# Optimization experiments

Hardware: AMD Instinct MI355X
Metric: run time of the kernel (lower is better)

Reference implementation:

```python
import jax, jax.numpy as jnp
import numpy as np

B, N, DIM, HEADS = 2048, 64, 256, 8
WH = WW = 8  # window size; N = WH*WW


def _buffers():
    # continuous relative coords table [1, 2*WH-1, 2*WW-1, 2], log-scaled as in Swin-V2
    rh = np.arange(-(WH - 1), WH, dtype=np.float32)
    rw = np.arange(-(WW - 1), WW, dtype=np.float32)
    t = np.stack(np.meshgrid(rh, rw, indexing='ij'), axis=-1)[None]
    t[..., 0] /= (WH - 1)
    t[..., 1] /= (WW - 1)
    t *= 8.0
    t = np.sign(t) * np.log2(np.abs(t) + 1.0) / np.log2(8.0)
    # relative position index [N, N]
    ch, cw = np.arange(WH), np.arange(WW)
    coords = np.stack(np.meshgrid(ch, cw, indexing='ij')).reshape(2, -1)
    rel = (coords[:, :, None] - coords[:, None, :]).transpose(1, 2, 0)
    rel[..., 0] += WH - 1
    rel[..., 1] += WW - 1
    rel[..., 0] *= 2 * WW - 1
    idx = rel.sum(-1)
    return jnp.asarray(t, dtype=jnp.float32), jnp.asarray(idx, dtype=jnp.int32)


def setup_inputs() -> dict:
    key = jax.random.key(0)
    ks = jax.random.split(key, 8)
    tbl, idx = _buffers()
    return {
        'x': jax.random.normal(ks[0], (B, N, DIM), dtype=jnp.float32),
        'qkv_w': jax.random.normal(ks[1], (3 * DIM, DIM), dtype=jnp.float32) * 0.02,
        'q_bias': jnp.zeros((DIM,), dtype=jnp.float32),
        'v_bias': jnp.zeros((DIM,), dtype=jnp.float32),
        'scale': jnp.full((HEADS, 1, 1), np.log(10.0), dtype=jnp.float32),
        'cpb_w1': jax.random.normal(ks[2], (512, 2), dtype=jnp.float32) * 0.02,
        'cpb_b1': jnp.zeros((512,), dtype=jnp.float32),
        'cpb_w2': jax.random.normal(ks[3], (HEADS, 512), dtype=jnp.float32) * 0.02,
        'proj_w': jax.random.normal(ks[4], (DIM, DIM), dtype=jnp.float32) * 0.02,
        'proj_b': jnp.zeros((DIM,), dtype=jnp.float32),
        'rel_coords_table': tbl,
        'rel_pos_index': idx,
    }


def reference(x, qkv_w, q_bias, v_bias, scale, cpb_w1, cpb_b1, cpb_w2,
              proj_w, proj_b, rel_coords_table, rel_pos_index):
    b, n, c = x.shape
    h = scale.shape[0]
    d = c // h
    # qkv projection, bias = [q_bias, 0, v_bias]
    bias = jnp.concatenate([q_bias, jnp.zeros_like(v_bias), v_bias])
    qkv = x @ qkv_w.T + bias
    q, k, v = jnp.split(qkv, 3, axis=-1)
    to_heads = lambda t: t.reshape(b, n, h, d).transpose(0, 2, 1, 3)  # b h n d
    q, k, v = to_heads(q), to_heads(k), to_heads(v)
    # cosine attention: L2-normalize q, k (F.normalize eps=1e-12)
    l2n = lambda t: t / jnp.maximum(jnp.linalg.norm(t, axis=-1, keepdims=True), 1e-12)
    q, k = l2n(q), l2n(k)
    attn = jnp.einsum('bhnd,bhmd->bhnm', q, k)
    # clamped learnable log-temperature per head
    sc = jnp.exp(jnp.minimum(scale, jnp.log(jnp.float32(100.0))))  # [h,1,1]
    attn = attn * sc
    # continuous position bias: MLP(2->512->h), gathered by rel index, 16*sigmoid
    tbl = jax.nn.relu(rel_coords_table @ cpb_w1.T + cpb_b1) @ cpb_w2.T  # [1,15,15,h]
    tbl = tbl.reshape(-1, h)
    cpb = tbl[rel_pos_index.reshape(-1)].reshape(n, n, h).transpose(2, 0, 1)  # [h,n,n]
    attn = attn + 16.0 * jax.nn.sigmoid(cpb)[None]
    attn = jax.nn.softmax(attn, axis=-1)
    out = jnp.einsum('bhnm,bhmd->bhnd', attn, v)
    out = out.transpose(0, 2, 1, 3).reshape(b, n, c)
    return out @ proj_w.T + proj_b
```

## Files before the change

### kernel.cpp

```cpp
#include <hip/hip_runtime.h>
#include <stdint.h>

typedef unsigned short u16;
typedef unsigned int u32;
typedef short bf8_t __attribute__((ext_vector_type(8)));
typedef float f4_t  __attribute__((ext_vector_type(4)));
typedef float f16_t __attribute__((ext_vector_type(16)));

#define LOG2E 1.44269504088896340736f

static __device__ __forceinline__ u32 pkbf(float lo, float hi){
  u32 r; asm("v_cvt_pk_bf16_f32 %0, %1, %2" : "=v"(r) : "v"(lo), "v"(hi)); return r;
}

static __device__ __forceinline__ float pair_add(float v, bool hi5){
  union { float f; u32 u; } a; a.f = v;
  auto r = __builtin_amdgcn_permlane32_swap(a.u, a.u, false, false);
  union { u32 u; float f; } p; p.u = hi5 ? r[0] : r[1];
  return v + p.f;
}

static __device__ __forceinline__ void cvt_tile(const f16_t c, bf8_t& f0, bf8_t& f1){
  u32 p0 = pkbf(c[0], c[1]),  p1 = pkbf(c[2], c[3]);
  u32 p2 = pkbf(c[4], c[5]),  p3 = pkbf(c[6], c[7]);
  u32 p4 = pkbf(c[8], c[9]),  p5 = pkbf(c[10], c[11]);
  u32 p6 = pkbf(c[12], c[13]), p7 = pkbf(c[14], c[15]);
  auto r02 = __builtin_amdgcn_permlane32_swap(p0, p2, false, false);
  auto r13 = __builtin_amdgcn_permlane32_swap(p1, p3, false, false);
  auto r46 = __builtin_amdgcn_permlane32_swap(p4, p6, false, false);
  auto r57 = __builtin_amdgcn_permlane32_swap(p5, p7, false, false);
  union { u32 u[4]; bf8_t b; } x0, x1;
  x0.u[0] = r02[0]; x0.u[1] = r13[0]; x0.u[2] = r02[1]; x0.u[3] = r13[1];
  x1.u[0] = r46[0]; x1.u[1] = r57[0]; x1.u[2] = r46[1]; x1.u[3] = r57[1];
  f0 = x0.b; f1 = x1.b;
}

#define MFMA32(a, b, c) __builtin_amdgcn_mfma_f32_32x32x16_bf16(a, b, c, 0, 0, 0)


__global__ __launch_bounds__(256)
void prep_kernel(const float* __restrict__ qkvw, const float* __restrict__ projw,
                 const float* __restrict__ tab, const float* __restrict__ w1,
                 const float* __restrict__ b1, const float* __restrict__ w2,
                 u16* __restrict__ wpk, float* __restrict__ tbl){
  __shared__ float red[4][8];
  if (blockIdx.x < 128){
    int u = blockIdx.x * 256 + threadIdx.x;
    int hb  = u >> 10;
    int ks  = (u >> 6) & 15;
    int l5  = (u >> 5) & 1;
    int l31 = u & 31;
    int row = hb * 32 + l31, col = ks * 16 + l5 * 8;
    const float* src = (row < 768) ? (qkvw + (size_t)row * 256 + col)
                                   : (projw + (size_t)(row - 768) * 256 + col);
    float4 v0 = *reinterpret_cast<const float4*>(src);
    float4 v1 = *reinterpret_cast<const float4*>(src + 4);
    uint4 p;
    p.x = pkbf(v0.x, v0.y); p.y = pkbf(v0.z, v0.w);
    p.z = pkbf(v1.x, v1.y); p.w = pkbf(v1.z, v1.w);
    *reinterpret_cast<uint4*>(wpk + (size_t)u * 8) = p;
  } else {
    int i = blockIdx.x - 128;
    int tid = threadIdx.x;
    int wv = tid >> 6, lane = tid & 63;
    float c0 = tab[2*i], c1 = tab[2*i+1];
    int j0 = tid * 2;
    float4 w14 = *reinterpret_cast<const float4*>(w1 + 2*j0);
    float2 b12 = *reinterpret_cast<const float2*>(b1 + j0);
    float h0 = fmaxf(fmaf(c1, w14.y, fmaf(c0, w14.x, b12.x)), 0.f);
    float h1 = fmaxf(fmaf(c1, w14.w, fmaf(c0, w14.z, b12.y)), 0.f);
    float part[8];
    #pragma unroll
    for (int hh = 0; hh < 8; hh++){
      float2 w22 = *reinterpret_cast<const float2*>(w2 + hh*512 + j0);
      part[hh] = fmaf(h1, w22.y, h0 * w22.x);
    }
    #pragma unroll
    for (int hh = 0; hh < 8; hh++)
      #pragma unroll
      for (int off = 1; off < 64; off <<= 1)
        part[hh] += __shfl_xor(part[hh], off);
    if (lane == 0){
      #pragma unroll
      for (int hh = 0; hh < 8; hh++) red[wv][hh] = part[hh];
    }
    __syncthreads();
    if (tid < 8)
      tbl[i*8 + tid] = (red[0][tid] + red[1][tid]) + (red[2][tid] + red[3][tid]);
  }
}

__global__ void cpbgather_kernel(const float* __restrict__ tbl, const int* __restrict__ idx,
                                 const float* __restrict__ scale, float* __restrict__ biasF,
                                 float* __restrict__ scf){
  int u = blockIdx.x * blockDim.x + threadIdx.x;
  int rl   = u & 3;
  int lane = (u >> 2) & 63;
  int r4   = (u >> 8) & 3;
  int tile = (u >> 10) & 3;
  int hh   = (u >> 12) & 7;
  int qt = tile & 1, kt = tile >> 1;
  int query = 32*qt + (lane & 31);
  int key   = 32*kt + rl + 8*r4 + 4*(lane >> 5);
  int id = idx[query*64 + key];
  float xv = tbl[id*8 + hh];
  float s = 1.f / (1.f + expf(-xv));
  float qsh = expf(fminf(scale[hh], 4.6051701859880913680f)) * LOG2E;
  biasF[u] = 16.f * s * LOG2E - (qsh + 24.0f);
  if (u < 8) scf[u] = qsh;
}

#define XS 264

__global__ __launch_bounds__(512, 4)
void winattn_kernel(const float* __restrict__ x, const u16* __restrict__ wpk,
                    const float* __restrict__ qb, const float* __restrict__ vbias,
                    const float* __restrict__ biasF, const float* __restrict__ scf,
                    const float* __restrict__ projb, float* __restrict__ out){
  __shared__ u16 xlds[64 * XS];
  __shared__ u16 olds[64 * XS];

  const int b = blockIdx.x;
  const int t = threadIdx.x;
  const int w = t >> 6, lane = t & 63;
  const int l31 = lane & 31, l5 = lane >> 5;
  const bool hi5 = (l5 != 0);
  const int h = w;
  const int fragoff = l5 * 256 + l31 * 8;

  {
    const f4_t* xg = reinterpret_cast<const f4_t*>(x + (size_t)b * 16384);
    #pragma unroll
    for (int i = 0; i < 8; i++){
      int fi = t + 512 * i;
      f4_t v = __builtin_nontemporal_load(xg + fi);
      uint2 p; p.x = pkbf(v[0], v[1]); p.y = pkbf(v[2], v[3]);
      *reinterpret_cast<uint2*>(&xlds[(fi >> 6) * XS + (fi & 63) * 4]) = p;
    }
  }
  __syncthreads();

  bf8_t qf0, qf1, qf2, qf3;
  bf8_t kf0, kf1, kf2, kf3;
  bf8_t vf0, vf1, vf2, vf3;
  const float qs = scf[h];

  {
    f16_t cq0, cq1;
    #pragma unroll
    for (int r = 0; r < 16; r++){
      float bqr = qb[32*h + (r & 3) + 8*(r >> 2) + 4*l5];
      cq0[r] = bqr; cq1[r] = bqr;
    }
    const u16* wqf = wpk + (size_t)h * 8192 + fragoff;
    __builtin_amdgcn_s_setprio(1);
    #pragma unroll 4
    for (int ks = 0; ks < 16; ks++){
      const int ko = ks * 16 + 8 * l5;
      bf8_t aq  = *reinterpret_cast<const bf8_t*>(wqf + ks * 512);
      bf8_t bx0 = *reinterpret_cast<const bf8_t*>(&xlds[l31 * XS + ko]);
      bf8_t bx1 = *reinterpret_cast<const bf8_t*>(&xlds[(32 + l31) * XS + ko]);
      cq0 = MFMA32(aq, bx0, cq0);
      cq1 = MFMA32(aq, bx1, cq1);
    }
    __builtin_amdgcn_s_setprio(0);
    {
      float sq = 0.f;
      #pragma unroll
      for (int r = 0; r < 16; r++) sq = fmaf(cq0[r], cq0[r], sq);
      sq = pair_add(sq, hi5);
      float iq = qs * __builtin_amdgcn_rsqf(fmaxf(sq, 1e-24f));
      #pragma unroll
      for (int r = 0; r < 16; r++) cq0[r] *= iq;
      cvt_tile(cq0, qf0, qf1);
    }
    {
      float sq = 0.f;
      #pragma unroll
      for (int r = 0; r < 16; r++) sq = fmaf(cq1[r], cq1[r], sq);
      sq = pair_add(sq, hi5);
      float iq = qs * __builtin_amdgcn_rsqf(fmaxf(sq, 1e-24f));
      #pragma unroll
      for (int r = 0; r < 16; r++) cq1[r] *= iq;
      cvt_tile(cq1, qf2, qf3);
    }
  }

  {
    f16_t ck0, ck1;
    #pragma unroll
    for (int r = 0; r < 16; r++){ ck0[r] = 0.f; ck1[r] = 0.f; }
    const u16* wkf = wpk + (size_t)(8 + h) * 8192 + fragoff;
    __builtin_amdgcn_s_setprio(1);
    #pragma unroll 4
    for (int ks = 0; ks < 16; ks++){
      const int ko = ks * 16 + 8 * l5;
      bf8_t ak  = *reinterpret_cast<const bf8_t*>(wkf + ks * 512);
      bf8_t bx0 = *reinterpret_cast<const bf8_t*>(&xlds[l31 * XS + ko]);
      bf8_t bx1 = *reinterpret_cast<const bf8_t*>(&xlds[(32 + l31) * XS + ko]);
      ck0 = MFMA32(ak, bx0, ck0);
      ck1 = MFMA32(ak, bx1, ck1);
    }
    __builtin_amdgcn_s_setprio(0);
    {
      float sk = 0.f;
      #pragma unroll
      for (int r = 0; r < 16; r++) sk = fmaf(ck0[r], ck0[r], sk);
      sk = pair_add(sk, hi5);
      float ik = __builtin_amdgcn_rsqf(fmaxf(sk, 1e-24f));
      #pragma unroll
      for (int r = 0; r < 16; r++) ck0[r] *= ik;
      cvt_tile(ck0, kf0, kf1);
    }
    {
      float sk = 0.f;
      #pragma unroll
      for (int r = 0; r < 16; r++) sk = fmaf(ck1[r], ck1[r], sk);
      sk = pair_add(sk, hi5);
      float ik = __builtin_amdgcn_rsqf(fmaxf(sk, 1e-24f));
      #pragma unroll
      for (int r = 0; r < 16; r++) ck1[r] *= ik;
      cvt_tile(ck1, kf2, kf3);
    }
  }

  {
    f16_t cv0, cv1;
    float bv = vbias[32*h + l31];
    #pragma unroll
    for (int r = 0; r < 16; r++){ cv0[r] = bv; cv1[r] = bv; }
    const u16* wvf = wpk + (size_t)(16 + h) * 8192 + fragoff;
    __builtin_amdgcn_s_setprio(1);
    #pragma unroll 4
    for (int ks = 0; ks < 16; ks++){
      const int ko = ks * 16 + 8 * l5;
      bf8_t bw  = *reinterpret_cast<const bf8_t*>(wvf + ks * 512);
      bf8_t ax0 = *reinterpret_cast<const bf8_t*>(&xlds[l31 * XS + ko]);
      bf8_t ax1 = *reinterpret_cast<const bf8_t*>(&xlds[(32 + l31) * XS + ko]);
      cv0 = MFMA32(ax0, bw, cv0);
      cv1 = MFMA32(ax1, bw, cv1);
    }
    __builtin_amdgcn_s_setprio(0);
    cvt_tile(cv0, vf0, vf1);
    cvt_tile(cv1, vf2, vf3);
  }

  #pragma unroll
  for (int nt = 0; nt < 2; nt++){
    union { f16_t c; f4_t q[4]; } S0, S1;
    {
      const f4_t* bf0 = reinterpret_cast<const f4_t*>(biasF) + (h*4 + nt    ) * 256 + lane;
      const f4_t* bf1 = reinterpret_cast<const f4_t*>(biasF) + (h*4 + 2 + nt) * 256 + lane;
      #pragma unroll
      for (int r4 = 0; r4 < 4; r4++){ S0.q[r4] = bf0[r4 * 64]; S1.q[r4] = bf1[r4 * 64]; }
    }
    f16_t s0 = S0.c, s1 = S1.c;
    bf8_t qfa = nt ? qf2 : qf0, qfb = nt ? qf3 : qf1;
    __builtin_amdgcn_s_setprio(1);
    s0 = MFMA32(kf0, qfa, s0); s0 = MFMA32(kf1, qfb, s0);
    s1 = MFMA32(kf2, qfa, s1); s1 = MFMA32(kf3, qfb, s1);
    __builtin_amdgcn_s_setprio(0);
    #pragma unroll
    for (int r = 0; r < 16; r++){
      s0[r] = __builtin_amdgcn_exp2f(s0[r]);
      s1[r] = __builtin_amdgcn_exp2f(s1[r]);
    }
    float a0 = 0.f, a1 = 0.f, a2 = 0.f, a3 = 0.f;
    #pragma unroll
    for (int r4 = 0; r4 < 4; r4++){
      a0 += s0[4*r4 + 0] + s1[4*r4 + 0];
      a1 += s0[4*r4 + 1] + s1[4*r4 + 1];
      a2 += s0[4*r4 + 2] + s1[4*r4 + 2];
      a3 += s0[4*r4 + 3] + s1[4*r4 + 3];
    }
    float ssum = pair_add((a0 + a1) + (a2 + a3), hi5);
    float invr = __builtin_amdgcn_rcpf(ssum);
    bf8_t pf0, pf1, pf2, pf3;
    cvt_tile(s0, pf0, pf1);
    cvt_tile(s1, pf2, pf3);
    f16_t co;
    #pragma unroll
    for (int r = 0; r < 16; r++) co[r] = 0.f;
    __builtin_amdgcn_s_setprio(1);
    co = MFMA32(vf0, pf0, co); co = MFMA32(vf1, pf1, co);
    co = MFMA32(vf2, pf2, co); co = MFMA32(vf3, pf3, co);
    __builtin_amdgcn_s_setprio(0);
    #pragma unroll
    for (int r4 = 0; r4 < 4; r4++){
      uint2 p;
      p.x = pkbf(co[4*r4 + 0] * invr, co[4*r4 + 1] * invr);
      p.y = pkbf(co[4*r4 + 2] * invr, co[4*r4 + 3] * invr);
      *reinterpret_cast<uint2*>(&olds[(32*nt + l31) * XS + 32*h + 8*r4 + 4*l5]) = p;
    }
  }
  __syncthreads();

  {
    f16_t cp0, cp1;
    float pbv = projb[32*w + l31];
    #pragma unroll
    for (int r = 0; r < 16; r++){ cp0[r] = pbv; cp1[r] = pbv; }
    const u16* wpf = wpk + (size_t)(24 + w) * 8192 + fragoff;
    __builtin_amdgcn_s_setprio(1);
    #pragma unroll 4
    for (int ks = 0; ks < 16; ks++){
      const int ko = ks * 16 + 8 * l5;
      bf8_t bw = *reinterpret_cast<const bf8_t*>(wpf + ks * 512);
      bf8_t a0 = *reinterpret_cast<const bf8_t*>(&olds[l31 * XS + ko]);
      bf8_t a1 = *reinterpret_cast<const bf8_t*>(&olds[(32 + l31) * XS + ko]);
      cp0 = MFMA32(a0, bw, cp0);
      cp1 = MFMA32(a1, bw, cp1);
    }
    __builtin_amdgcn_s_setprio(0);
    float* og = out + (size_t)b * 16384;
    #pragma unroll
    for (int r = 0; r < 16; r++){
      int m = (r & 3) + 8*(r >> 2) + 4*l5;
      __builtin_nontemporal_store(cp0[r], &og[m * 256 + 32*w + l31]);
      __builtin_nontemporal_store(cp1[r], &og[(32 + m) * 256 + 32*w + l31]);
    }
  }
}

extern "C" void kernel_launch(void* const* d_in, const int* in_sizes, int n_in,
                              void* d_out, int out_size, void* d_ws, size_t ws_size,
                              hipStream_t stream){
  const float* x     = (const float*)d_in[0];
  const float* qkvw  = (const float*)d_in[1];
  const float* qb    = (const float*)d_in[2];
  const float* vb    = (const float*)d_in[3];
  const float* scale = (const float*)d_in[4];
  const float* w1    = (const float*)d_in[5];
  const float* b1    = (const float*)d_in[6];
  const float* w2    = (const float*)d_in[7];
  const float* pw    = (const float*)d_in[8];
  const float* pb    = (const float*)d_in[9];
  const float* tab   = (const float*)d_in[10];
  const int*   idx   = (const int*)d_in[11];
  float* out = (float*)d_out;

  char* ws = (char*)d_ws;
  u16*   wpkp = (u16*)ws;
  float* bias = (float*)(ws + 524288);
  float* tbl  = (float*)(ws + 655360);
  float* scfp = (float*)(ws + 662560);

  hipLaunchKernelGGL(prep_kernel,     dim3(353), dim3(256), 0, stream,
                     qkvw, pw, tab, w1, b1, w2, wpkp, tbl);
  hipLaunchKernelGGL(cpbgather_kernel,dim3(128), dim3(256), 0, stream, tbl, idx, scale, bias, scfp);
  hipLaunchKernelGGL(winattn_kernel,  dim3(2048), dim3(512), 0, stream,
                     x, wpkp, qb, vb, bias, scfp, pb, out);
}
```

Measured before the change: 115.5 us.

## Stream weight fragments through per-wave LDS rings with async global-to-LDS DMA

Weight fragments for the Q, K, V and output projections are no longer loaded straight from global memory into registers. Each wave now streams them into its own 4-slot LDS ring using global_load_lds, keeping three k-steps in flight with explicit vmcnt waits. The first slots for the next projection are issued before the current phase's epilogue, and the ring sits in whichever LDS buffer is idle at that point. An extra barrier is added before the attention phase so the output buffer can be reused; the cost is more LDS traffic and tight hand-counted waits that depend on the order loads are issued.

New measurement: 245.4 us. +112.5%, slower.

```diff
diff --git a/kernel.cpp b/kernel.cpp
--- a/kernel.cpp
+++ b/kernel.cpp
@@ -36,6 +36,34 @@
 }
 
 #define MFMA32(a, b, c) __builtin_amdgcn_mfma_f32_32x32x16_bf16(a, b, c, 0, 0, 0)
+
+static __device__ __forceinline__ void dma16(const u16* g, u16* l){
+  __builtin_amdgcn_global_load_lds(
+      (const __attribute__((address_space(1))) u32*)g,
+      (__attribute__((address_space(3))) u32*)l,
+      16, 0, 0);
+}
+
+#define WAITV(N) do { asm volatile("s_waitcnt vmcnt(" #N ")" ::: "memory"); \
+                      __builtin_amdgcn_sched_barrier(0); } while(0)
+
+#define WITER(ks, N, WA) \
+  { WAITV(N); \
+    bf8_t wf = *reinterpret_cast<const bf8_t*>(ring + (((ks)&3)*512) + fragoff); \
+    const int ko = (ks)*16 + 8*l5; \
+    bf8_t x0 = *reinterpret_cast<const bf8_t*>(&xt[l31*XS + ko]); \
+    bf8_t x1 = *reinterpret_cast<const bf8_t*>(&xt[(32+l31)*XS + ko]); \
+    if (WA){ c0 = MFMA32(wf, x0, c0); c1 = MFMA32(wf, x1, c1); } \
+    else   { c0 = MFMA32(x0, wf, c0); c1 = MFMA32(x1, wf, c1); } \
+    if ((ks)+3 < 16) dma16(wsrc + ((ks)+3)*512, ring + (((ks)+3)&3)*512); }
+
+#define WLOOP(WA) \
+  WITER(0,2,WA) WITER(1,2,WA) WITER(2,2,WA) WITER(3,2,WA) WITER(4,2,WA) \
+  WITER(5,2,WA) WITER(6,2,WA) WITER(7,2,WA) WITER(8,2,WA) WITER(9,2,WA) \
+  WITER(10,2,WA) WITER(11,2,WA) WITER(12,2,WA) WITER(13,2,WA) WITER(14,1,WA) WITER(15,0,WA)
+
+#define WPRO() do { dma16(wsrc, ring); dma16(wsrc + 512, ring + 512); \
+                    dma16(wsrc + 1024, ring + 1024); } while(0)
 
 
 __global__ __launch_bounds__(256)
@@ -128,7 +156,16 @@
   const int h = w;
   const int fragoff = l5 * 256 + l31 * 8;
 
-  {
+  u16* ringO = &olds[w * 2048];
+  u16* ringX = &xlds[w * 2048];
+  const u16* wq_src = wpk + (size_t)h * 8192 + fragoff;
+  const u16* wk_src = wpk + (size_t)(8 + h) * 8192 + fragoff;
+  const u16* wv_src = wpk + (size_t)(16 + h) * 8192 + fragoff;
+  const u16* wp_src = wpk + (size_t)(24 + w) * 8192 + fragoff;
+
+  {
+    const u16* wsrc = wq_src; u16* ring = ringO;
+    WPRO();
     const f4_t* xg = reinterpret_cast<const f4_t*>(x + (size_t)b * 16384);
     #pragma unroll
     for (int i = 0; i < 8; i++){
@@ -146,105 +183,85 @@
   const float qs = scf[h];
 
   {
-    f16_t cq0, cq1;
+    f16_t c0, c1;
     #pragma unroll
     for (int r = 0; r < 16; r++){
       float bqr = qb[32*h + (r & 3) + 8*(r >> 2) + 4*l5];
-      cq0[r] = bqr; cq1[r] = bqr;
-    }
-    const u16* wqf = wpk + (size_t)h * 8192 + fragoff;
-    __builtin_amdgcn_s_setprio(1);
-    #pragma unroll 4
-    for (int ks = 0; ks < 16; ks++){
-      const int ko = ks * 16 + 8 * l5;
-      bf8_t aq  = *reinterpret_cast<const bf8_t*>(wqf + ks * 512);
-      bf8_t bx0 = *reinterpret_cast<const bf8_t*>(&xlds[l31 * XS + ko]);
-      bf8_t bx1 = *reinterpret_cast<const bf8_t*>(&xlds[(32 + l31) * XS + ko]);
-      cq0 = MFMA32(aq, bx0, cq0);
-      cq1 = MFMA32(aq, bx1, cq1);
-    }
-    __builtin_amdgcn_s_setprio(0);
+      c0[r] = bqr; c1[r] = bqr;
+    }
+    const u16* wsrc = wq_src; u16* ring = ringO; const u16* xt = xlds;
+    __builtin_amdgcn_s_setprio(1);
+    WLOOP(1)
+    __builtin_amdgcn_s_setprio(0);
+    { const u16* wsrc = wk_src; u16* ring = ringO; WPRO(); }
     {
       float sq = 0.f;
       #pragma unroll
-      for (int r = 0; r < 16; r++) sq = fmaf(cq0[r], cq0[r], sq);
+      for (int r = 0; r < 16; r++) sq = fmaf(c0[r], c0[r], sq);
       sq = pair_add(sq, hi5);
       float iq = qs * __builtin_amdgcn_rsqf(fmaxf(sq, 1e-24f));
       #pragma unroll
-      for (int r = 0; r < 16; r++) cq0[r] *= iq;
-      cvt_tile(cq0, qf0, qf1);
+      for (int r = 0; r < 16; r++) c0[r] *= iq;
+      cvt_tile(c0, qf0, qf1);
     }
     {
       float sq = 0.f;
       #pragma unroll
-      for (int r = 0; r < 16; r++) sq = fmaf(cq1[r], cq1[r], sq);
+      for (int r = 0; r < 16; r++) sq = fmaf(c1[r], c1[r], sq);
       sq = pair_add(sq, hi5);
       float iq = qs * __builtin_amdgcn_rsqf(fmaxf(sq, 1e-24f));
       #pragma unroll
-      for (int r = 0; r < 16; r++) cq1[r] *= iq;
-      cvt_tile(cq1, qf2, qf3);
-    }
-  }
-
-  {
-    f16_t ck0, ck1;
-    #pragma unroll
-    for (int r = 0; r < 16; r++){ ck0[r] = 0.f; ck1[r] = 0.f; }
-    const u16* wkf = wpk + (size_t)(8 + h) * 8192 + fragoff;
-    __builtin_amdgcn_s_setprio(1);
-    #pragma unroll 4
-    for (int ks = 0; ks < 16; ks++){
-      const int ko = ks * 16 + 8 * l5;
-      bf8_t ak  = *reinterpret_cast<const bf8_t*>(wkf + ks * 512);
-      bf8_t bx0 = *reinterpret_cast<const bf8_t*>(&xlds[l31 * XS + ko]);
-      bf8_t bx1 = *reinterpret_cast<const bf8_t*>(&xlds[(32 + l31) * XS + ko]);
-      ck0 = MFMA32(ak, bx0, ck0);
-      ck1 = MFMA32(ak, bx1, ck1);
-    }
-    __builtin_amdgcn_s_setprio(0);
+      for (int r = 0; r < 16; r++) c1[r] *= iq;
+      cvt_tile(c1, qf2, qf3);
+    }
+  }
+
+  {
+    f16_t c0, c1;
+    #pragma unroll
+    for (int r = 0; r < 16; r++){ c0[r] = 0.f; c1[r] = 0.f; }
+    const u16* wsrc = wk_src; u16* ring = ringO; const u16* xt = xlds;
+    __builtin_amdgcn_s_setprio(1);
+    WLOOP(1)
+    __builtin_amdgcn_s_setprio(0);
+    { const u16* wsrc = wv_src; u16* ring = ringO; WPRO(); }
     {
       float sk = 0.f;
       #pragma unroll
-      for (int r = 0; r < 16; r++) sk = fmaf(ck0[r], ck0[r], sk);
+      for (int r = 0; r < 16; r++) sk = fmaf(c0[r], c0[r], sk);
       sk = pair_add(sk, hi5);
       float ik = __builtin_amdgcn_rsqf(fmaxf(sk, 1e-24f));
       #pragma unroll
-      for (int r = 0; r < 16; r++) ck0[r] *= ik;
-      cvt_tile(ck0, kf0, kf1);
+      for (int r = 0; r < 16; r++) c0[r] *= ik;
+      cvt_tile(c0, kf0, kf1);
     }
     {
       float sk = 0.f;
       #pragma unroll
-      for (int r = 0; r < 16; r++) sk = fmaf(ck1[r], ck1[r], sk);
+      for (int r = 0; r < 16; r++) sk = fmaf(c1[r], c1[r], sk);
       sk = pair_add(sk, hi5);
       float ik = __builtin_amdgcn_rsqf(fmaxf(sk, 1e-24f));
       #pragma unroll
-      for (int r = 0; r < 16; r++) ck1[r] *= ik;
-      cvt_tile(ck1, kf2, kf3);
-    }
-  }
-
-  {
-    f16_t cv0, cv1;
+      for (int r = 0; r < 16; r++) c1[r] *= ik;
+      cvt_tile(c1, kf2, kf3);
+    }
+  }
+
+  {
+    f16_t c0, c1;
     float bv = vbias[32*h + l31];
     #pragma unroll
-    for (int r = 0; r < 16; r++){ cv0[r] = bv; cv1[r] = bv; }
-    const u16* wvf = wpk + (size_t)(16 + h) * 8192 + fragoff;
-    __builtin_amdgcn_s_setprio(1);
-    #pragma unroll 4
-    for (int ks = 0; ks < 16; ks++){
-      const int ko = ks * 16 + 8 * l5;
-      bf8_t bw  = *reinterpret_cast<const bf8_t*>(wvf + ks * 512);
-      bf8_t ax0 = *reinterpret_cast<const bf8_t*>(&xlds[l31 * XS + ko]);
-      bf8_t ax1 = *reinterpret_cast<const bf8_t*>(&xlds[(32 + l31) * XS + ko]);
-      cv0 = MFMA32(ax0, bw, cv0);
-      cv1 = MFMA32(ax1, bw, cv1);
-    }
-    __builtin_amdgcn_s_setprio(0);
-    cvt_tile(cv0, vf0, vf1);
-    cvt_tile(cv1, vf2, vf3);
-  }
-
+    for (int r = 0; r < 16; r++){ c0[r] = bv; c1[r] = bv; }
+    const u16* wsrc = wv_src; u16* ring = ringO; const u16* xt = xlds;
+    __builtin_amdgcn_s_setprio(1);
+    WLOOP(0)
+    __builtin_amdgcn_s_setprio(0);
+    cvt_tile(c0, vf0, vf1);
+    cvt_tile(c1, vf2, vf3);
+  }
+  __syncthreads();
+
+  { const u16* wsrc = wp_src; u16* ring = ringX; WPRO(); }
   #pragma unroll
   for (int nt = 0; nt < 2; nt++){
     union { f16_t c; f4_t q[4]; } S0, S1;
@@ -296,28 +313,20 @@
   __syncthreads();
 
   {
-    f16_t cp0, cp1;
+    f16_t c0, c1;
     float pbv = projb[32*w + l31];
     #pragma unroll
-    for (int r = 0; r < 16; r++){ cp0[r] = pbv; cp1[r] = pbv; }
-    const u16* wpf = wpk + (size_t)(24 + w) * 8192 + fragoff;
-    __builtin_amdgcn_s_setprio(1);
-    #pragma unroll 4
-    for (int ks = 0; ks < 16; ks++){
-      const int ko = ks * 16 + 8 * l5;
-      bf8_t bw = *reinterpret_cast<const bf8_t*>(wpf + ks * 512);
-      bf8_t a0 = *reinterpret_cast<const bf8_t*>(&olds[l31 * XS + ko]);
-      bf8_t a1 = *reinterpret_cast<const bf8_t*>(&olds[(32 + l31) * XS + ko]);
-      cp0 = MFMA32(a0, bw, cp0);
-      cp1 = MFMA32(a1, bw, cp1);
-    }
+    for (int r = 0; r < 16; r++){ c0[r] = pbv; c1[r] = pbv; }
+    const u16* wsrc = wp_src; u16* ring = ringX; const u16* xt = olds;
+    __builtin_amdgcn_s_setprio(1);
+    WLOOP(0)
     __builtin_amdgcn_s_setprio(0);
     float* og = out + (size_t)b * 16384;
     #pragma unroll
     for (int r = 0; r < 16; r++){
       int m = (r & 3) + 8*(r >> 2) + 4*l5;
-      __builtin_nontemporal_store(cp0[r], &og[m * 256 + 32*w + l31]);
-      __builtin_nontemporal_store(cp1[r], &og[(32 + m) * 256 + 32*w + l31]);
+      __builtin_nontemporal_store(c0[r], &og[m * 256 + 32*w + l31]);
+      __builtin_nontemporal_store(c1[r], &og[(32 + m) * 256 + 32*w + l31]);
     }
   }
 }
```
